# Kernel optimization log

Measured on AMD Instinct MI355X. Metric: run time of the kernel, lower is better.

Reference implementation:

```python
import jax, jax.numpy as jnp
import numpy as np

B, N, D_IN, D_OUT = 2, 2048, 2048, 2048
H, G = 16, 4            # num_heads, n_kv_groups
HD = D_OUT // H         # head_dim = 128
REP = H // G            # query heads per kv head = 4


def setup_inputs() -> dict:
    key = jax.random.key(0)
    ks = jax.random.split(key, 6)
    s = lambda fan_in: 1.0 / np.sqrt(fan_in)
    return {
        "x": jax.random.normal(ks[0], (B, N, D_IN), jnp.float32),
        "Wq": jax.random.normal(ks[1], (D_IN, D_OUT), jnp.float32) * s(D_IN),
        "Wk": jax.random.normal(ks[2], (D_IN, G * HD), jnp.float32) * s(D_IN),
        "Wv": jax.random.normal(ks[3], (D_IN, G * HD), jnp.float32) * s(D_IN),
        "Wo": jax.random.normal(ks[4], (D_OUT, D_OUT), jnp.float32) * s(D_OUT),
        "bo": jnp.zeros((D_OUT,), jnp.float32),
    }


def reference(x, Wq, Wk, Wv, Wo, bo):
    b, n, _ = x.shape
    # projections
    q = (x @ Wq).reshape(b, n, G, REP, HD)   # query heads grouped: h = g*REP + r
    k = (x @ Wk).reshape(b, n, G, HD)
    v = (x @ Wv).reshape(b, n, G, HD)
    # grouped attention scores; KV broadcast over REP instead of repeat_kv
    scores = jnp.einsum('bqgrd,bkgd->bgrqk', q, k)  # [b,G,REP,N,N]
    causal = jnp.tril(jnp.ones((n, n), bool))       # allowed positions
    scores = jnp.where(causal, scores, -jnp.inf)
    w = jax.nn.softmax(scores / np.float32(np.sqrt(HD)), axis=-1)
    ctx = jnp.einsum('bgrqk,bkgd->bqgrd', w, v).reshape(b, n, D_OUT)
    return ctx @ Wo + bo
```

## Files before the change

kernel.cpp:

```cpp
#include <hip/hip_runtime.h>
#include <stdint.h>

typedef __attribute__((ext_vector_type(8))) __bf16 bf16x8;
typedef __attribute__((ext_vector_type(4))) float f32x4;
typedef __attribute__((ext_vector_type(16))) float f32x16;
typedef __attribute__((ext_vector_type(4))) short short4v;
typedef __attribute__((ext_vector_type(4))) unsigned uint4v;

static constexpr int SEQ  = 2048;
static constexpr int DQKV = 3072;
static constexpr int HD   = 128;

__device__ __forceinline__ short f2bf(float f) {
  unsigned u = __builtin_bit_cast(unsigned, f);
  u += 0x7fffu + ((u >> 16) & 1u);
  return (short)(u >> 16);
}

__device__ __forceinline__ unsigned pack2(float a, float b) {
  return (unsigned)(unsigned short)f2bf(a) | ((unsigned)(unsigned short)f2bf(b) << 16);
}

__device__ __forceinline__ void gl_lds16(const void* g, void* l) {
  __builtin_amdgcn_global_load_lds(
      (const __attribute__((address_space(1))) void*)g,
      (__attribute__((address_space(3))) void*)l, 16, 0, 0);
}

__global__ __launch_bounds__(256)
void prep_kernel(const float* __restrict__ x, const float* __restrict__ Wq,
                 const float* __restrict__ Wk, const float* __restrict__ Wv,
                 const float* __restrict__ Wo,
                 short* __restrict__ xb, short* __restrict__ WqkvT,
                 short* __restrict__ WoT) {
  int blk = blockIdx.x, tid = threadIdx.x;
  if (blk < 8192) {
    int i = blk * 256 + tid;
    float4 v = reinterpret_cast<const float4*>(x)[i];
    short4v o;
    o[0] = f2bf(v.x); o[1] = f2bf(v.y); o[2] = f2bf(v.z); o[3] = f2bf(v.w);
    *reinterpret_cast<short4v*>(xb + (size_t)i * 4) = o;
    return;
  }
  blk -= 8192;
  __shared__ float tile[32][33];
  const float* in; short* out; int C, bx, by;
  if (blk < 4096)      { in = Wq; out = WqkvT;                     C = 2048; bx = blk & 63; by = blk >> 6; }
  else if (blk < 5120) { int t = blk - 4096; in = Wk; out = WqkvT + (size_t)2048 * 2048; C = 512; bx = t & 15; by = t >> 4; }
  else if (blk < 6144) { int t = blk - 5120; in = Wv; out = WqkvT + (size_t)2560 * 2048; C = 512; bx = t & 15; by = t >> 4; }
  else                 { int t = blk - 6144; in = Wo; out = WoT;   C = 2048; bx = t & 63; by = t >> 6; }
  const int R = 2048;
  int c0 = bx * 32, r0 = by * 32, tx = tid & 31, ty = tid >> 5;
  for (int i = 0; i < 4; i++)
    tile[ty + i * 8][tx] = in[(size_t)(r0 + ty + i * 8) * C + c0 + tx];
  __syncthreads();
  for (int i = 0; i < 4; i++)
    out[(size_t)(c0 + ty + i * 8) * R + r0 + tx] = f2bf(tile[tx][ty + i * 8]);
}

__global__ __launch_bounds__(256) void transpose_v_kernel(const short* __restrict__ qkv,
                                                          short* __restrict__ vT) {
  __shared__ short tile[32][33];
  int n0 = blockIdx.x * 32, c0 = blockIdx.y * 32, b = blockIdx.z;
  int tx = threadIdx.x & 31, ty = threadIdx.x >> 5;
  for (int i = 0; i < 4; i++)
    tile[ty + i * 8][tx] = qkv[(size_t)(b * SEQ + n0 + ty + i * 8) * DQKV + 2560 + c0 + tx];
  __syncthreads();
  for (int i = 0; i < 4; i++)
    vT[(size_t)(b * 512 + c0 + ty + i * 8) * SEQ + n0 + tx] = tile[tx][ty + i * 8];
}

template <int F32OUT>
__global__ __launch_bounds__(256)
void gemm_bt_kernel(const short* __restrict__ A, const short* __restrict__ BT,
                    void* __restrict__ Cout, const float* __restrict__ bias,
                    int M, int N, int K, int qcols, float qscale) {
  __shared__ __align__(16) short As[8192];
  __shared__ __align__(16) short Bs[8192];
  const int tid = threadIdx.x, lane = tid & 63, w = tid >> 6;
  const int l15 = lane & 15, quad = lane >> 4, q8 = quad * 8;
  const int row0 = blockIdx.y * 128, col0 = blockIdx.x * 128;
  const int wm = (w >> 1) * 64, wn = (w & 1) * 64;
  f32x4 acc[4][4] = {};
  const short* ga0 = A  + (size_t)(row0 + w * 16 + (lane >> 2)) * K + (lane & 3) * 8;
  const short* gb0 = BT + (size_t)(col0 + w * 16 + (lane >> 2)) * K + (lane & 3) * 8;
  for (int kt = 0; kt < K; kt += 64) {
    for (int s = 0; s < 2; s++) {
      gl_lds16(ga0 + kt + s * 32,                  As + s * 4096 + w * 512);
      gl_lds16(ga0 + (size_t)64 * K + kt + s * 32, As + s * 4096 + 2048 + w * 512);
      gl_lds16(gb0 + kt + s * 32,                  Bs + s * 4096 + w * 512);
      gl_lds16(gb0 + (size_t)64 * K + kt + s * 32, Bs + s * 4096 + 2048 + w * 512);
    }
    __syncthreads();
    for (int s = 0; s < 2; s++) {
      bf16x8 af[4], bfr[4];
      for (int i = 0; i < 4; i++)
        af[i] = *reinterpret_cast<const bf16x8*>(As + s * 4096 + (wm + i * 16 + l15) * 32 + q8);
      for (int j = 0; j < 4; j++)
        bfr[j] = *reinterpret_cast<const bf16x8*>(Bs + s * 4096 + (wn + j * 16 + l15) * 32 + q8);
      for (int i = 0; i < 4; i++)
        for (int j = 0; j < 4; j++)
          acc[i][j] = __builtin_amdgcn_mfma_f32_16x16x32_bf16(af[i], bfr[j], acc[i][j], 0, 0, 0);
    }
    __syncthreads();
  }
  if (F32OUT) {
    float* C = (float*)Cout;
    for (int j = 0; j < 4; j++) {
      int col = col0 + wn + j * 16 + l15;
      float bv = bias[col];
      for (int i = 0; i < 4; i++)
        for (int r = 0; r < 4; r++)
          C[(size_t)(row0 + wm + i * 16 + quad * 4 + r) * N + col] = acc[i][j][r] + bv;
    }
  } else {
    short* C = (short*)Cout;
    for (int j = 0; j < 4; j++) {
      int col = col0 + wn + j * 16 + l15;
      float sc = (col < qcols) ? qscale : 1.0f;
      for (int i = 0; i < 4; i++)
        for (int r = 0; r < 4; r++)
          C[(size_t)(row0 + wm + i * 16 + quad * 4 + r) * N + col] = f2bf(acc[i][j][r] * sc);
    }
  }
}

__global__ __launch_bounds__(256, 2)
void attn_kernel(const short* __restrict__ qkv, const short* __restrict__ vT,
                 short* __restrict__ ctx) {
  __shared__ __align__(16) short Ks[2 * 8192];
  __shared__ __align__(16) short Vs[2 * 8192];
  __shared__ __align__(16) float Oex[2048];
  __shared__ float lbuf[4 * 32];
  const int tid = threadIdx.x, lane = tid & 63, w = tid >> 6;
  const int l31 = lane & 31, hi = lane >> 5;
  const int qh = w & 1, kh = w >> 1;
  const int idx = blockIdx.x;
  const int p = idx >> 5, h = (idx >> 1) & 15, b = idx & 1, g = h >> 2;
  const int qtA = 31 - p, qtB = p;
  const int lenA = qtA + 1, total = lenA + qtB + 1;

  auto stage = [&](int buf, int kt) {
    const short* gk = qkv + (size_t)(b * SEQ + kt * 64) * DQKV + 2048 + g * HD;
#pragma unroll
    for (int s = 0; s < 4; s++) {
      const int r = w * 16 + s * 4 + (lane >> 4);
      gl_lds16(gk + (size_t)r * DQKV + ((lane & 15) ^ (r & 7)) * 8,
               Ks + buf * 8192 + (w * 16 + s * 4) * 128);
    }
    const short* gv = vT + (size_t)(b * 512 + g * HD) * SEQ + kt * 64;
#pragma unroll
    for (int s = 0; s < 4; s++) {
      const int r = w * 32 + s * 8 + (lane >> 3);
      gl_lds16(gv + (size_t)r * SEQ + ((lane & 7) ^ (r & 7)) * 8,
               Vs + buf * 8192 + (w * 32 + s * 8) * 64);
    }
  };

  bf16x8 qf[8];
  f32x16 o_acc[4] = {};
  float lsum = 0.f;

  stage(0, 0);
  for (int t = 0; t < total; t++) {
    const int seg = (t >= lenA);
    const int kt = seg ? (t - lenA) : t;
    const int qt = seg ? qtB : qtA;
    const int cur = t & 1;
    __syncthreads();

    if (t + 1 < total) {
      const int nkt = (t + 1 >= lenA) ? (t + 1 - lenA) : (t + 1);
      stage(cur ^ 1, nkt);
    }
    __builtin_amdgcn_sched_barrier(0);

    if (t == 0 || t == lenA) {
      const short* gq = qkv + (size_t)(b * SEQ + qt * 64 + qh * 32 + l31) * DQKV + h * HD + hi * 8;
#pragma unroll
      for (int d = 0; d < 8; d++) qf[d] = *reinterpret_cast<const bf16x8*>(gq + d * 16);
    }

    const short* Kb = Ks + cur * 8192;
    f32x16 sa0 = {}, sa1 = {};
    __builtin_amdgcn_s_setprio(1);
#pragma unroll
    for (int d = 0; d < 4; d++) {
      bf16x8 kf0 = *reinterpret_cast<const bf16x8*>(
          Kb + (kh * 32 + l31) * 128 + (((2 * d + hi) ^ (l31 & 7)) * 8));
      bf16x8 kf1 = *reinterpret_cast<const bf16x8*>(
          Kb + (kh * 32 + l31) * 128 + (((2 * (d + 4) + hi) ^ (l31 & 7)) * 8));
      sa0 = __builtin_amdgcn_mfma_f32_32x32x16_bf16(kf0, qf[d], sa0, 0, 0, 0);
      sa1 = __builtin_amdgcn_mfma_f32_32x32x16_bf16(kf1, qf[d + 4], sa1, 0, 0, 0);
    }
    __builtin_amdgcn_s_setprio(0);
    f32x16 sa = sa0 + sa1;

    if (kt == qt) {
      const int q = qh * 32 + l31;
#pragma unroll
      for (int r = 0; r < 16; r++)
        if (kh * 32 + (r & 3) + 8 * (r >> 2) + 4 * hi > q) sa[r] = -1e38f;
    }

    float ps[16];
#pragma unroll
    for (int r = 0; r < 16; r++) ps[r] = exp2f(sa[r]);
#pragma unroll
    for (int r = 0; r < 16; r++) lsum += ps[r];
    unsigned ub[4][2];
#pragma unroll
    for (int j = 0; j < 4; j++) {
      unsigned a0 = __builtin_bit_cast(unsigned, ps[4 * j + 0]);
      unsigned a1 = __builtin_bit_cast(unsigned, ps[4 * j + 1]);
      unsigned a2 = __builtin_bit_cast(unsigned, ps[4 * j + 2]);
      unsigned a3 = __builtin_bit_cast(unsigned, ps[4 * j + 3]);
      ub[j][0] = (a0 >> 16) | (a1 & 0xffff0000u);
      ub[j][1] = (a2 >> 16) | (a3 & 0xffff0000u);
    }
    bf16x8 pfrag[2];
#pragma unroll
    for (int sub = 0; sub < 2; sub++) {
      auto s0 = __builtin_amdgcn_permlane32_swap((int)ub[2 * sub][0], (int)ub[2 * sub + 1][0], false, false);
      auto s1 = __builtin_amdgcn_permlane32_swap((int)ub[2 * sub][1], (int)ub[2 * sub + 1][1], false, false);
      uint4v uu;
      uu[0] = (unsigned)s0[0]; uu[1] = (unsigned)s1[0];
      uu[2] = (unsigned)s0[1]; uu[3] = (unsigned)s1[1];
      pfrag[sub] = __builtin_bit_cast(bf16x8, uu);
    }

    const short* Vb = Vs + cur * 8192;
    __builtin_amdgcn_s_setprio(1);
#pragma unroll
    for (int dt = 0; dt < 4; dt++) {
#pragma unroll
      for (int sub = 0; sub < 2; sub++) {
        const int kc = kh * 4 + sub * 2 + hi;
        bf16x8 vf = *reinterpret_cast<const bf16x8*>(
            Vb + (dt * 32 + l31) * 64 + ((kc ^ (l31 & 7)) * 8));
        o_acc[dt] = __builtin_amdgcn_mfma_f32_32x32x16_bf16(vf, pfrag[sub], o_acc[dt], 0, 0, 0);
      }
    }
    __builtin_amdgcn_s_setprio(0);

    if (kt == qt) {
      float lp = lsum + __shfl_xor(lsum, 32, 64);
      if (lane < 32) lbuf[w * 32 + l31] = lp;
      float invl = 0.f;
      const size_t row = (size_t)(b * SEQ + qt * 64 + qh * 32 + l31);
#pragma unroll
      for (int dt = 0; dt < 4; dt++) {
        if (w >= 2) {
          float* oex = Oex + (w - 2) * 1024;
#pragma unroll
          for (int rq = 0; rq < 4; rq++) {
            f32x4 vv = {o_acc[dt][4 * rq + 0], o_acc[dt][4 * rq + 1],
                        o_acc[dt][4 * rq + 2], o_acc[dt][4 * rq + 3]};
            *reinterpret_cast<f32x4*>(oex + (rq * 64 + lane) * 4) = vv;
          }
        }
        __syncthreads();
        if (w < 2) {
          if (dt == 0) invl = 1.f / (lp + lbuf[(w ^ 2) * 32 + l31]);
          const float* oex = Oex + w * 1024;
#pragma unroll
          for (int rq = 0; rq < 4; rq++) {
            f32x4 vv = *reinterpret_cast<const f32x4*>(oex + (rq * 64 + lane) * 4);
            float e0 = (o_acc[dt][4 * rq + 0] + vv[0]) * invl;
            float e1 = (o_acc[dt][4 * rq + 1] + vv[1]) * invl;
            float e2 = (o_acc[dt][4 * rq + 2] + vv[2]) * invl;
            float e3 = (o_acc[dt][4 * rq + 3] + vv[3]) * invl;
            uint2 dd = make_uint2(pack2(e0, e1), pack2(e2, e3));
            *reinterpret_cast<uint2*>(ctx + row * 2048 + h * HD + dt * 32 + rq * 8 + hi * 4) = dd;
          }
        }
        __syncthreads();
      }
#pragma unroll
      for (int dt = 0; dt < 4; dt++)
#pragma unroll
        for (int e = 0; e < 16; e++) o_acc[dt][e] = 0.f;
      lsum = 0.f;
    }
  }
}

extern "C" void kernel_launch(void* const* d_in, const int* in_sizes, int n_in,
                              void* d_out, int out_size, void* d_ws, size_t ws_size,
                              hipStream_t stream) {
  const float* x  = (const float*)d_in[0];
  const float* Wq = (const float*)d_in[1];
  const float* Wk = (const float*)d_in[2];
  const float* Wv = (const float*)d_in[3];
  const float* Wo = (const float*)d_in[4];
  const float* bo = (const float*)d_in[5];
  float* out = (float*)d_out;

  const float sc2 = 0.08838834764831845f * 1.4426950408889634f;

  short* xb    = (short*)d_ws;
  short* WqkvT = xb    + (size_t)4096 * 2048;
  short* WoT   = WqkvT + (size_t)3072 * 2048;
  short* qkv   = WoT   + (size_t)2048 * 2048;
  short* vT    = qkv   + (size_t)4096 * 3072;
  short* ctx   = vT    + (size_t)1024 * 2048;

  prep_kernel<<<dim3(18432), dim3(256), 0, stream>>>(x, Wq, Wk, Wv, Wo, xb, WqkvT, WoT);
  gemm_bt_kernel<0><<<dim3(24, 32), dim3(256), 0, stream>>>(xb, WqkvT, qkv, nullptr,
                                                            4096, 3072, 2048, 2048, sc2);
  transpose_v_kernel<<<dim3(64, 16, 2), dim3(256), 0, stream>>>(qkv, vT);
  attn_kernel<<<dim3(512), dim3(256), 0, stream>>>(qkv, vT, ctx);
  gemm_bt_kernel<1><<<dim3(16, 32), dim3(256), 0, stream>>>(ctx, WoT, out, bo,
                                                            4096, 2048, 2048, 0, 1.0f);
}
```

Baseline: 281.3 us.

## Pre-swizzle K and V in global memory at 8-byte granularity, hoist V LDS loads

The LDS bank swizzle moves out of the attention staging addresses and into the producers. The QKV GEMM epilogue writes the K columns XOR-permuted in 4-element units, and the V transpose kernel (now 64-row tiles) writes vT pre-permuted, so the attention kernel copies contiguous rows into LDS. Fragments are then read as two 8-byte loads at finer-grained swizzled offsets to cut bank conflicts. V fragments are now loaded right after the QK MFMAs so their LDS latency overlaps the softmax, which costs more live registers.

```diff
diff --git a/kernel.cpp b/kernel.cpp
--- a/kernel.cpp
+++ b/kernel.cpp
@@ -25,6 +25,10 @@
   __builtin_amdgcn_global_load_lds(
       (const __attribute__((address_space(1))) void*)g,
       (__attribute__((address_space(3))) void*)l, 16, 0, 0);
+}
+
+__device__ __forceinline__ int vswz(int d) {
+  return (d & 15) ^ ((d & 16) >> 2) ^ ((d & 2) << 2);
 }
 
 __global__ __launch_bounds__(256)
@@ -60,14 +64,19 @@
 
 __global__ __launch_bounds__(256) void transpose_v_kernel(const short* __restrict__ qkv,
                                                           short* __restrict__ vT) {
-  __shared__ short tile[32][33];
-  int n0 = blockIdx.x * 32, c0 = blockIdx.y * 32, b = blockIdx.z;
+  __shared__ short tile[64][33];
+  int n0 = blockIdx.x * 64, c0 = blockIdx.y * 32, b = blockIdx.z;
   int tx = threadIdx.x & 31, ty = threadIdx.x >> 5;
-  for (int i = 0; i < 4; i++)
+  for (int i = 0; i < 8; i++)
     tile[ty + i * 8][tx] = qkv[(size_t)(b * SEQ + n0 + ty + i * 8) * DQKV + 2560 + c0 + tx];
   __syncthreads();
-  for (int i = 0; i < 4; i++)
-    vT[(size_t)(b * 512 + c0 + ty + i * 8) * SEQ + n0 + tx] = tile[tx][ty + i * 8];
+  int k6 = threadIdx.x & 63, dq = threadIdx.x >> 6;
+  for (int j = 0; j < 8; j++) {
+    int dl = dq + j * 4;
+    int dv = c0 + dl;
+    int ks = ((((k6 >> 2) ^ vswz(dv)) & 15) << 2) | (k6 & 3);
+    vT[(size_t)(b * 512 + dv) * SEQ + n0 + ks] = tile[k6][dl];
+  }
 }
 
 template <int F32OUT>
@@ -118,9 +127,14 @@
     for (int j = 0; j < 4; j++) {
       int col = col0 + wn + j * 16 + l15;
       float sc = (col < qcols) ? qscale : 1.0f;
+      const bool kreg = (col >= 2048) && (col < 2560);
+      const int cbase = col & ~127, cu = (col & 127) >> 2, cl = col & 3;
       for (int i = 0; i < 4; i++)
-        for (int r = 0; r < 4; r++)
-          C[(size_t)(row0 + wm + i * 16 + quad * 4 + r) * N + col] = f2bf(acc[i][j][r] * sc);
+        for (int r = 0; r < 4; r++) {
+          int row = row0 + wm + i * 16 + quad * 4 + r;
+          int cc = kreg ? (cbase | ((cu ^ (row & 31)) << 2) | cl) : col;
+          C[(size_t)row * N + cc] = f2bf(acc[i][j][r] * sc);
+        }
     }
   }
 }
@@ -139,22 +153,40 @@
   const int p = idx >> 5, h = (idx >> 1) & 15, b = idx & 1, g = h >> 2;
   const int qtA = 31 - p, qtB = p;
   const int lenA = qtA + 1, total = lenA + qtB + 1;
+  const int hv = vswz(l31);
 
   auto stage = [&](int buf, int kt) {
     const short* gk = qkv + (size_t)(b * SEQ + kt * 64) * DQKV + 2048 + g * HD;
 #pragma unroll
     for (int s = 0; s < 4; s++) {
       const int r = w * 16 + s * 4 + (lane >> 4);
-      gl_lds16(gk + (size_t)r * DQKV + ((lane & 15) ^ (r & 7)) * 8,
+      gl_lds16(gk + (size_t)r * DQKV + (lane & 15) * 8,
                Ks + buf * 8192 + (w * 16 + s * 4) * 128);
     }
     const short* gv = vT + (size_t)(b * 512 + g * HD) * SEQ + kt * 64;
 #pragma unroll
     for (int s = 0; s < 4; s++) {
       const int r = w * 32 + s * 8 + (lane >> 3);
-      gl_lds16(gv + (size_t)r * SEQ + ((lane & 7) ^ (r & 7)) * 8,
+      gl_lds16(gv + (size_t)r * SEQ + (lane & 7) * 8,
                Vs + buf * 8192 + (w * 32 + s * 8) * 64);
     }
+  };
+
+  auto ldK = [&](const short* Kb, int kr, int u) -> bf16x8 {
+    const short* rowp = Kb + kr * 128;
+    const int po = (u ^ l31) * 4;
+    uint2 r1 = *reinterpret_cast<const uint2*>(rowp + po);
+    uint2 r2 = *reinterpret_cast<const uint2*>(rowp + (po ^ 4));
+    uint4v uu; uu[0] = r1.x; uu[1] = r1.y; uu[2] = r2.x; uu[3] = r2.y;
+    return __builtin_bit_cast(bf16x8, uu);
+  };
+  auto ldV = [&](const short* Vb, int dr, int u) -> bf16x8 {
+    const short* rowp = Vb + dr * 64;
+    const int po = (u ^ hv) * 4;
+    uint2 r1 = *reinterpret_cast<const uint2*>(rowp + po);
+    uint2 r2 = *reinterpret_cast<const uint2*>(rowp + (po ^ 4));
+    uint4v uu; uu[0] = r1.x; uu[1] = r1.y; uu[2] = r2.x; uu[3] = r2.y;
+    return __builtin_bit_cast(bf16x8, uu);
   };
 
   bf16x8 qf[8];
@@ -182,20 +214,26 @@
     }
 
     const short* Kb = Ks + cur * 8192;
+    const short* Vb = Vs + cur * 8192;
     f32x16 sa0 = {}, sa1 = {};
     __builtin_amdgcn_s_setprio(1);
 #pragma unroll
     for (int d = 0; d < 4; d++) {
-      bf16x8 kf0 = *reinterpret_cast<const bf16x8*>(
-          Kb + (kh * 32 + l31) * 128 + (((2 * d + hi) ^ (l31 & 7)) * 8));
-      bf16x8 kf1 = *reinterpret_cast<const bf16x8*>(
-          Kb + (kh * 32 + l31) * 128 + (((2 * (d + 4) + hi) ^ (l31 & 7)) * 8));
+      bf16x8 kf0 = ldK(Kb, kh * 32 + l31, 4 * d + 2 * hi);
+      bf16x8 kf1 = ldK(Kb, kh * 32 + l31, 4 * (d + 4) + 2 * hi);
       sa0 = __builtin_amdgcn_mfma_f32_32x32x16_bf16(kf0, qf[d], sa0, 0, 0, 0);
       sa1 = __builtin_amdgcn_mfma_f32_32x32x16_bf16(kf1, qf[d + 4], sa1, 0, 0, 0);
     }
     __builtin_amdgcn_s_setprio(0);
+
+    bf16x8 vf[4][2];
+#pragma unroll
+    for (int dt = 0; dt < 4; dt++)
+#pragma unroll
+      for (int sub = 0; sub < 2; sub++)
+        vf[dt][sub] = ldV(Vb, dt * 32 + l31, (kh * 2 + sub) * 4 + hi * 2);
+
     f32x16 sa = sa0 + sa1;
-
     if (kt == qt) {
       const int q = qh * 32 + l31;
 #pragma unroll
@@ -229,18 +267,12 @@
       pfrag[sub] = __builtin_bit_cast(bf16x8, uu);
     }
 
-    const short* Vb = Vs + cur * 8192;
     __builtin_amdgcn_s_setprio(1);
 #pragma unroll
-    for (int dt = 0; dt < 4; dt++) {
-#pragma unroll
-      for (int sub = 0; sub < 2; sub++) {
-        const int kc = kh * 4 + sub * 2 + hi;
-        bf16x8 vf = *reinterpret_cast<const bf16x8*>(
-            Vb + (dt * 32 + l31) * 64 + ((kc ^ (l31 & 7)) * 8));
-        o_acc[dt] = __builtin_amdgcn_mfma_f32_32x32x16_bf16(vf, pfrag[sub], o_acc[dt], 0, 0, 0);
-      }
-    }
+    for (int dt = 0; dt < 4; dt++)
+#pragma unroll
+      for (int sub = 0; sub < 2; sub++)
+        o_acc[dt] = __builtin_amdgcn_mfma_f32_32x32x16_bf16(vf[dt][sub], pfrag[sub], o_acc[dt], 0, 0, 0);
     __builtin_amdgcn_s_setprio(0);
 
     if (kt == qt) {
@@ -308,7 +340,7 @@
   prep_kernel<<<dim3(18432), dim3(256), 0, stream>>>(x, Wq, Wk, Wv, Wo, xb, WqkvT, WoT);
   gemm_bt_kernel<0><<<dim3(24, 32), dim3(256), 0, stream>>>(xb, WqkvT, qkv, nullptr,
                                                             4096, 3072, 2048, 2048, sc2);
-  transpose_v_kernel<<<dim3(64, 16, 2), dim3(256), 0, stream>>>(qkv, vT);
+  transpose_v_kernel<<<dim3(32, 16, 2), dim3(256), 0, stream>>>(qkv, vT);
   attn_kernel<<<dim3(512), dim3(256), 0, stream>>>(qkv, vT, ctx);
   gemm_bt_kernel<1><<<dim3(16, 32), dim3(256), 0, stream>>>(ctx, WoT, out, bo,
                                                             4096, 2048, 2048, 0, 1.0f);
```

Result: slower. 311.4 us (+10.7%).
